# Kernel optimization log

Measured on AMD Instinct MI355X. Metric: run time of the kernel, lower is better.

The kernel has to match this reference:

```python
import jax, jax.numpy as jnp
import numpy as np

N = 50000      # nodes
E2 = 400000    # undirected edges
E = 2 * E2     # directed edges (each undirected edge in both directions)
DIN = 512      # input feature dim
DH = 128       # MLP hidden
C = 8          # num classes / BP channels


def setup_inputs() -> dict:
    key = jax.random.key(0)
    ks = jax.random.split(key, 9)
    x = jax.random.normal(ks[0], (N, DIN), jnp.float32)
    src0 = jax.random.randint(ks[1], (E2,), 0, N)
    dst0 = jax.random.randint(ks[2], (E2,), 0, N)
    # symmetric directed edge list: row 0 = source j, row 1 = target i
    edge_index = jnp.stack([jnp.concatenate([src0, dst0]),
                            jnp.concatenate([dst0, src0])])
    w0 = jax.random.uniform(ks[3], (E2,), jnp.float32, 0.5, 1.5)
    edge_weight = jnp.concatenate([w0, w0])  # reverse edge shares weight
    # edge_rv[e] = index of the reverse of edge e
    edge_rv = jnp.concatenate([jnp.arange(E2) + E2, jnp.arange(E2)])
    W1 = jax.random.normal(ks[4], (DIN, DH), jnp.float32) * 0.05
    b1 = jnp.zeros((DH,), jnp.float32)
    W2 = jax.random.normal(ks[5], (DH, C), jnp.float32) * 0.05
    b2 = jnp.zeros((C,), jnp.float32)
    param = jax.random.normal(ks[6], (C, C), jnp.float32) * 0.1
    return {"x": x, "edge_index": edge_index, "edge_weight": edge_weight,
            "edge_rv": edge_rv, "W1": W1, "b1": b1, "W2": W2, "b2": b2,
            "param": param, "K": 5}


def log_normalize(log_x):
    return log_x - jax.nn.logsumexp(log_x, axis=-1, keepdims=True)


def reference(x, edge_index, edge_weight, edge_rv, W1, b1, W2, b2, param, K):
    # MLP transform + LogSoftmax -> initial log-beliefs [N, C]
    h = jax.nn.relu(x @ W1 + b1)
    log_b0 = jax.nn.log_softmax(h @ W2 + b2, axis=-1)

    # learn_H=True: logH = logsigmoid(param + param^T), [C, C]
    logH = jax.nn.log_sigmoid(param + param.T)
    src, dst = edge_index[0], edge_index[1]
    # per-edge coupling matrix [E, C, C]
    logC = edge_weight[:, None, None] * logH[None, :, :]

    log_b = log_b0
    log_msg = None
    for _ in range(K):
        x_j = log_b[src]                       # gather source beliefs [E, C]
        if log_msg is not None:
            x_j = x_j - log_msg[edge_rv]       # remove reverse message
        # tropical-semiring matvec in log domain: logsumexp over source channel
        log_msg = log_normalize(jax.nn.logsumexp(x_j[:, :, None] + logC, axis=1))
        agg = jax.ops.segment_sum(log_msg, dst, num_segments=N)  # scatter-add
        log_b = log_normalize(log_b0 + agg)
    return log_b
```

## Files before the change

kernel.cpp:

```cpp
#include <hip/hip_runtime.h>
#include <hip/hip_bf16.h>
#include <math.h>

#define NN 50000
#define EE 800000
#define DINK 512
#define DHK 128
#define CK 8
#define KIT 5
#define NBLKS 196

typedef __attribute__((ext_vector_type(8))) short short8;
typedef __attribute__((ext_vector_type(4))) float f32x4;

__device__ __forceinline__ unsigned short f2bf(float f) {
    union { float f; unsigned int u; } v;
    v.f = f;
    unsigned int u = v.u;
    unsigned int r = (u + 0x7FFFu + ((u >> 16) & 1u)) >> 16;
    return (unsigned short)r;
}
__device__ __forceinline__ float bfu2f(unsigned int lo16) {
    union { unsigned int u; float f; } v;
    v.u = lo16 << 16;
    return v.f;
}

__global__ __launch_bounds__(64) void logH_kernel(const float* __restrict__ param,
                                                  float* __restrict__ logH) {
    int t = threadIdx.x;
    int i = t >> 3, j = t & 7;
    float z = param[i * 8 + j] + param[j * 8 + i];
    logH[t] = fminf(z, 0.0f) - log1pf(expf(-fabsf(z)));
}

__global__ __launch_bounds__(256) void w1t_kernel(const float* __restrict__ W1,
                                                  unsigned short* __restrict__ W1t) {
    int idx = blockIdx.x * 256 + threadIdx.x;
    int n = idx >> 9;
    int k = idx & 511;
    W1t[idx] = f2bf(W1[(size_t)k * DHK + n]);
}

__global__ __launch_bounds__(256) void mlp_mfma_kernel(
    const float* __restrict__ x, const unsigned short* __restrict__ W1t,
    const float* __restrict__ b1, const float* __restrict__ W2,
    const float* __restrict__ b2, float* __restrict__ logb0) {
    __shared__ unsigned short hs[128 * 136];
    __shared__ float W2s[128 * 8];
    __shared__ float b1s[128];
    __shared__ float b2s[8];

    const int tid = threadIdx.x;
    const int wave = tid >> 6;
    const int lane = tid & 63;
    const int q = lane >> 4;
    const int lm = lane & 15;
    const int wm = wave >> 1, wn = wave & 1;
    const int n0 = blockIdx.x * 128;

    if (tid < 128) b1s[tid] = b1[tid];
    if (tid < 8) b2s[tid] = b2[tid];
    {
        int i = tid * 4;
        *(float4*)&W2s[i] = *(const float4*)&W2[i];
    }
    __syncthreads();

    const float* xptr[4];
#pragma unroll
    for (int mt = 0; mt < 4; ++mt) {
        int r = n0 + wm * 64 + mt * 16 + lm;
        if (r > NN - 1) r = NN - 1;
        xptr[mt] = x + (size_t)r * DINK + q * 8;
    }
    const unsigned short* bptr[4];
#pragma unroll
    for (int nt = 0; nt < 4; ++nt) {
        int c = wn * 64 + nt * 16 + lm;
        bptr[nt] = W1t + (size_t)c * DINK + q * 8;
    }

    f32x4 acc[4][4];
#pragma unroll
    for (int mt = 0; mt < 4; ++mt)
#pragma unroll
        for (int nt = 0; nt < 4; ++nt) acc[mt][nt] = (f32x4){0.f, 0.f, 0.f, 0.f};

    float4 ar[4][2];
    short8 bc[4];
#pragma unroll
    for (int mt = 0; mt < 4; ++mt) {
        ar[mt][0] = *(const float4*)(xptr[mt]);
        ar[mt][1] = *(const float4*)(xptr[mt] + 4);
    }
#pragma unroll
    for (int nt = 0; nt < 4; ++nt) bc[nt] = *(const short8*)(bptr[nt]);

#pragma unroll
    for (int k0 = 32; k0 <= DINK; k0 += 32) {
        float4 ar2[4][2];
        short8 b2f[4];
        if (k0 < DINK) {
#pragma unroll
            for (int mt = 0; mt < 4; ++mt) {
                ar2[mt][0] = *(const float4*)(xptr[mt] + k0);
                ar2[mt][1] = *(const float4*)(xptr[mt] + k0 + 4);
            }
#pragma unroll
            for (int nt = 0; nt < 4; ++nt)
                b2f[nt] = *(const short8*)(bptr[nt] + k0);
        }
        short8 af[4];
#pragma unroll
        for (int mt = 0; mt < 4; ++mt) {
            union { short8 s; __hip_bfloat162 h[4]; } cv;
            cv.h[0] = __float22bfloat162_rn(make_float2(ar[mt][0].x, ar[mt][0].y));
            cv.h[1] = __float22bfloat162_rn(make_float2(ar[mt][0].z, ar[mt][0].w));
            cv.h[2] = __float22bfloat162_rn(make_float2(ar[mt][1].x, ar[mt][1].y));
            cv.h[3] = __float22bfloat162_rn(make_float2(ar[mt][1].z, ar[mt][1].w));
            af[mt] = cv.s;
        }
#pragma unroll
        for (int mt = 0; mt < 4; ++mt)
#pragma unroll
            for (int nt = 0; nt < 4; ++nt)
                acc[mt][nt] = __builtin_amdgcn_mfma_f32_16x16x32_bf16(
                    af[mt], bc[nt], acc[mt][nt], 0, 0, 0);
        if (k0 < DINK) {
#pragma unroll
            for (int mt = 0; mt < 4; ++mt) {
                ar[mt][0] = ar2[mt][0];
                ar[mt][1] = ar2[mt][1];
            }
#pragma unroll
            for (int nt = 0; nt < 4; ++nt) bc[nt] = b2f[nt];
        }
    }

#pragma unroll
    for (int nt = 0; nt < 4; ++nt) {
        int j = wn * 64 + nt * 16 + lm;
        float bj = b1s[j];
#pragma unroll
        for (int mt = 0; mt < 4; ++mt) {
            int rbase = wm * 64 + mt * 16 + q * 4;
#pragma unroll
            for (int r = 0; r < 4; ++r) {
                float h = fmaxf(acc[mt][nt][r] + bj, 0.0f);
                hs[(rbase + r) * 136 + j] = f2bf(h);
            }
        }
    }
    __syncthreads();

    int row = tid >> 1;
    int half = tid & 1;
    const unsigned short* hp = &hs[row * 136 + half * 64];
    float p[8] = {0.f, 0.f, 0.f, 0.f, 0.f, 0.f, 0.f, 0.f};
#pragma unroll
    for (int ch = 0; ch < 8; ++ch) {
        uint4 c4 = *(const uint4*)(hp + ch * 8);
        unsigned int uu[4] = {c4.x, c4.y, c4.z, c4.w};
#pragma unroll
        for (int p2 = 0; p2 < 4; ++p2) {
            float h0 = bfu2f(uu[p2] & 0xFFFFu);
            float h1 = bfu2f(uu[p2] >> 16);
            int j = half * 64 + ch * 8 + p2 * 2;
            const float* w0 = &W2s[j * 8];
            const float* w1 = &W2s[(j + 1) * 8];
#pragma unroll
            for (int c = 0; c < 8; ++c) p[c] = fmaf(h0, w0[c], p[c]);
#pragma unroll
            for (int c = 0; c < 8; ++c) p[c] = fmaf(h1, w1[c], p[c]);
        }
    }
#pragma unroll
    for (int c = 0; c < 8; ++c) p[c] += __shfl_xor(p[c], 1, 64);
    int grow = n0 + row;
    if (half == 0 && grow < NN) {
        float v[8];
        float mx = -1e30f;
#pragma unroll
        for (int c = 0; c < 8; ++c) {
            v[c] = p[c] + b2s[c];
            mx = fmaxf(mx, v[c]);
        }
        float s = 0.0f;
#pragma unroll
        for (int c = 0; c < 8; ++c) s += expf(v[c] - mx);
        float ln = mx + logf(s);
        float4* p0 = (float4*)&logb0[(size_t)grow * 8];
        p0[0] = make_float4(v[0] - ln, v[1] - ln, v[2] - ln, v[3] - ln);
        p0[1] = make_float4(v[4] - ln, v[5] - ln, v[6] - ln, v[7] - ln);
    }
}


__global__ __launch_bounds__(256) void deg_kernel(const int* __restrict__ dst,
                                                  int* __restrict__ cnt) {
    int e = blockIdx.x * 256 + threadIdx.x;
    if (e < EE) atomicAdd(&cnt[dst[e]], 1);
}

__global__ __launch_bounds__(256) void scan_partial_kernel(
    const int* __restrict__ cnt, int* __restrict__ partial) {
    __shared__ int sd[256];
    int t = threadIdx.x;
    int i = blockIdx.x * 256 + t;
    sd[t] = (i < NN) ? cnt[i] : 0;
    __syncthreads();
#pragma unroll
    for (int s = 128; s > 0; s >>= 1) {
        if (t < s) sd[t] += sd[t + s];
        __syncthreads();
    }
    if (t == 0) partial[blockIdx.x] = sd[0];
}

__global__ __launch_bounds__(256) void scan_tops_kernel(
    const int* __restrict__ partial, int* __restrict__ tops) {
    __shared__ int sd[256];
    int t = threadIdx.x;
    sd[t] = (t < NBLKS) ? partial[t] : 0;
    __syncthreads();
#pragma unroll
    for (int s = 1; s < 256; s <<= 1) {
        int a = sd[t];
        int b = (t >= s) ? sd[t - s] : 0;
        __syncthreads();
        sd[t] = a + b;
        __syncthreads();
    }
    if (t < NBLKS) tops[t] = (t > 0) ? sd[t - 1] : 0;
}

__global__ __launch_bounds__(256) void scan_write_kernel(
    const int* __restrict__ cnt, const int* __restrict__ tops,
    int* __restrict__ off) {
    __shared__ int sd[256];
    int t = threadIdx.x;
    int i = blockIdx.x * 256 + t;
    int v = (i < NN) ? cnt[i] : 0;
    sd[t] = v;
    __syncthreads();
#pragma unroll
    for (int s = 1; s < 256; s <<= 1) {
        int a = sd[t];
        int b = (t >= s) ? sd[t - s] : 0;
        __syncthreads();
        sd[t] = a + b;
        __syncthreads();
    }
    if (i < NN) off[i] = tops[blockIdx.x] + sd[t] - v;
    if (i == NN - 1) off[NN] = EE;
}

__global__ __launch_bounds__(256) void pos_kernel(
    const int* __restrict__ src, const int* __restrict__ dst,
    const float* __restrict__ ew, const int* __restrict__ off,
    int* __restrict__ cnt, int* __restrict__ pos,
    int2* __restrict__ perm_sw, int* __restrict__ perm_dst) {
    int e = blockIdx.x * 256 + threadIdx.x;
    if (e >= EE) return;
    int d = dst[e];
    int p = off[d] + atomicAdd(&cnt[d], 1);
    pos[e] = p;
    int2 sw;
    sw.x = src[e];
    sw.y = __float_as_int(ew[e]);
    perm_sw[p] = sw;
    perm_dst[p] = d;
}

__global__ __launch_bounds__(256) void rvpos_kernel(const int* __restrict__ rv,
                                                    const int* __restrict__ pos,
                                                    int* __restrict__ perm_rvp) {
    int e = blockIdx.x * 256 + threadIdx.x;
    if (e >= EE) return;
    perm_rvp[pos[e]] = pos[rv[e]];
}

__global__ __launch_bounds__(256) void init_xin_kernel(
    const int2* __restrict__ perm_sw, const float* __restrict__ logb0,
    float* __restrict__ xin, float* __restrict__ perm_w) {
    int p = blockIdx.x * 256 + threadIdx.x;
    if (p >= EE) return;
    int2 sw = perm_sw[p];
    perm_w[p] = __int_as_float(sw.y);
    const float4* pb = (const float4*)&logb0[(size_t)sw.x * 8];
    float4 a = pb[0], b = pb[1];
    float4* po = (float4*)&xin[(size_t)p * 8];
    po[0] = a;
    po[1] = b;
}


__global__ __launch_bounds__(256) void edge_msg_kernel(
    const float* __restrict__ perm_w, const float* __restrict__ logH,
    const float* __restrict__ xin, float* __restrict__ msg_out) {
    __shared__ float lH[64];
    if (threadIdx.x < 64) lH[threadIdx.x] = logH[threadIdx.x];
    __syncthreads();
    int p = blockIdx.x * 256 + threadIdx.x;
    if (p >= EE) return;

    float w = perm_w[p];
    const float4* pb = (const float4*)&xin[(size_t)p * 8];
    float4 v0 = pb[0], v1 = pb[1];
    float xj[8] = {v0.x, v0.y, v0.z, v0.w, v1.x, v1.y, v1.z, v1.w};

    float M = xj[0];
#pragma unroll
    for (int c = 1; c < 8; ++c) M = fmaxf(M, xj[c]);
#pragma unroll
    for (int c = 0; c < 8; ++c) xj[c] -= M;

    float mg[8];
#pragma unroll
    for (int c2 = 0; c2 < 8; ++c2) {
        float ssum = 0.0f;
#pragma unroll
        for (int c1 = 0; c1 < 8; ++c1)
            ssum += __expf(fmaf(w, lH[c1 * 8 + c2], xj[c1]));
        mg[c2] = M + __logf(ssum);
    }

    float4* po = (float4*)&msg_out[(size_t)p * 8];
    po[0] = make_float4(mg[0], mg[1], mg[2], mg[3]);
    po[1] = make_float4(mg[4], mg[5], mg[6], mg[7]);
}

__global__ __launch_bounds__(256) void node_belief_kernel(
    const float* __restrict__ logb0, const int* __restrict__ off,
    const float* __restrict__ msg, float* __restrict__ belief,
    float* __restrict__ out, int write_out) {
    int t = blockIdx.x * 256 + threadIdx.x;
    int n = t >> 3;
    int c = t & 7;
    if (n >= NN) return;
    int j0 = off[n], j1 = off[n + 1];
    float a = logb0[(size_t)n * 8 + c];
    for (int j = j0; j < j1; ++j) a += msg[(size_t)j * 8 + c];
    float mx = a;
#pragma unroll
    for (int s = 1; s < 8; s <<= 1) mx = fmaxf(mx, __shfl_xor(mx, s, 8));
    float ex = __expf(a - mx);
    float sum = ex;
#pragma unroll
    for (int s = 1; s < 8; s <<= 1) sum += __shfl_xor(sum, s, 8);
    float v = a - (mx + __logf(sum));
    if (write_out) out[(size_t)n * 8 + c] = v;
    else belief[(size_t)n * 8 + c] = v;
}

__global__ __launch_bounds__(256) void edge_scatter_kernel(
    const int* __restrict__ perm_dst, const int* __restrict__ perm_rvp,
    const float* __restrict__ belief, const float* __restrict__ msg,
    float* __restrict__ xin) {
    int p = blockIdx.x * 256 + threadIdx.x;
    if (p >= EE) return;
    int d = perm_dst[p];
    int r = perm_rvp[p];
    const float4* pb = (const float4*)&belief[(size_t)d * 8];
    float4 b0 = pb[0], b1 = pb[1];
    const float4* pm = (const float4*)&msg[(size_t)p * 8];
    float4 m0 = pm[0], m1 = pm[1];
    float4* po = (float4*)&xin[(size_t)r * 8];
    po[0] = make_float4(b0.x - m0.x, b0.y - m0.y, b0.z - m0.z, b0.w - m0.w);
    po[1] = make_float4(b1.x - m1.x, b1.y - m1.y, b1.z - m1.z, b1.w - m1.w);
}

extern "C" void kernel_launch(void* const* d_in, const int* in_sizes, int n_in,
                              void* d_out, int out_size, void* d_ws, size_t ws_size,
                              hipStream_t stream) {
    const float* x = (const float*)d_in[0];
    const int* ei = (const int*)d_in[1];
    const float* ew = (const float*)d_in[2];
    const int* rv = (const int*)d_in[3];
    const float* W1 = (const float*)d_in[4];
    const float* b1 = (const float*)d_in[5];
    const float* W2 = (const float*)d_in[6];
    const float* b2 = (const float*)d_in[7];
    const float* param = (const float*)d_in[8];
    float* out = (float*)d_out;

    const int* src = ei;
    const int* dst = ei + EE;

    float* wsf = (float*)d_ws;
    float* logH = wsf;
    float* logb0 = logH + 64;
    float* belief = logb0 + (size_t)NN * 8;
    float* msg = belief + (size_t)NN * 8;
    float* xin = msg + (size_t)EE * 8;
    float* perm_w = xin + (size_t)EE * 8;
    int* off = (int*)(perm_w + EE);
    int2* perm_sw = (int2*)(off + (NN + 1));
    int* perm_rvp = (int*)(perm_sw + EE);
    int* perm_dst = perm_rvp + EE;
    unsigned short* W1t = (unsigned short*)(perm_dst + EE);
    int* pos = (int*)xin;
    int* cnt = pos + EE;
    int* partial = cnt + NN;
    int* tops = partial + NBLKS;

    logH_kernel<<<1, 64, 0, stream>>>(param, logH);
    w1t_kernel<<<256, 256, 0, stream>>>(W1, W1t);
    mlp_mfma_kernel<<<(NN + 127) / 128, 256, 0, stream>>>(x, W1t, b1, W2, b2,
                                                          logb0);

    const int EB = (EE + 255) / 256;

    hipMemsetAsync(cnt, 0, (size_t)NN * sizeof(int), stream);
    deg_kernel<<<EB, 256, 0, stream>>>(dst, cnt);
    scan_partial_kernel<<<NBLKS, 256, 0, stream>>>(cnt, partial);
    scan_tops_kernel<<<1, 256, 0, stream>>>(partial, tops);
    scan_write_kernel<<<NBLKS, 256, 0, stream>>>(cnt, tops, off);
    hipMemsetAsync(cnt, 0, (size_t)NN * sizeof(int), stream);
    pos_kernel<<<EB, 256, 0, stream>>>(src, dst, ew, off, cnt, pos, perm_sw,
                                       perm_dst);
    rvpos_kernel<<<EB, 256, 0, stream>>>(rv, pos, perm_rvp);
    init_xin_kernel<<<EB, 256, 0, stream>>>(perm_sw, logb0, xin, perm_w);

    const int NB8 = (NN * 8 + 255) / 256;
    for (int it = 0; it < KIT; ++it) {
        int last = (it == KIT - 1) ? 1 : 0;
        edge_msg_kernel<<<EB, 256, 0, stream>>>(perm_w, logH, xin, msg);
        node_belief_kernel<<<NB8, 256, 0, stream>>>(logb0, off, msg, belief,
                                                    out, last);
        if (!last)
            edge_scatter_kernel<<<EB, 256, 0, stream>>>(perm_dst, perm_rvp,
                                                        belief, msg, xin);
    }
}
```

Measured before the change: 503.9 us.

## Fuse belief normalization with reverse-message scatter and drop init/prep kernels

Merges the node belief kernel and the edge scatter kernel into one per-node-block kernel. Each block keeps its 32 normalized beliefs in shared memory and scatters belief minus message to the reverse-edge slots for its contiguous CSR edge range. It also drops the init_xin kernel and the perm_w array by having the first edge_msg iteration gather logb0 directly and read the weight from perm_sw, and it merges the logH and W1 transpose prep kernels into one launch. The aim is fewer launches and no round-trip of beliefs through global memory. The cost is that the scatter loop's work per block varies with node degree, which can unbalance blocks.

```diff
diff --git a/kernel.cpp b/kernel.cpp
--- a/kernel.cpp
+++ b/kernel.cpp
@@ -9,6 +9,7 @@
 #define CK 8
 #define KIT 5
 #define NBLKS 196
+#define NPB 32
 
 typedef __attribute__((ext_vector_type(8))) short short8;
 typedef __attribute__((ext_vector_type(4))) float f32x4;
@@ -26,20 +27,20 @@
     return v.f;
 }
 
-__global__ __launch_bounds__(64) void logH_kernel(const float* __restrict__ param,
-                                                  float* __restrict__ logH) {
-    int t = threadIdx.x;
-    int i = t >> 3, j = t & 7;
-    float z = param[i * 8 + j] + param[j * 8 + i];
-    logH[t] = fminf(z, 0.0f) - log1pf(expf(-fabsf(z)));
-}
-
-__global__ __launch_bounds__(256) void w1t_kernel(const float* __restrict__ W1,
-                                                  unsigned short* __restrict__ W1t) {
-    int idx = blockIdx.x * 256 + threadIdx.x;
-    int n = idx >> 9;
-    int k = idx & 511;
-    W1t[idx] = f2bf(W1[(size_t)k * DHK + n]);
+__global__ __launch_bounds__(256) void prep_kernel(
+    const float* __restrict__ W1, const float* __restrict__ param,
+    unsigned short* __restrict__ W1t, float* __restrict__ logH) {
+    if (blockIdx.x < 256) {
+        int idx = blockIdx.x * 256 + threadIdx.x;
+        int n = idx >> 9;
+        int k = idx & 511;
+        W1t[idx] = f2bf(W1[(size_t)k * DHK + n]);
+    } else if (threadIdx.x < 64) {
+        int t = threadIdx.x;
+        int i = t >> 3, j = t & 7;
+        float z = param[i * 8 + j] + param[j * 8 + i];
+        logH[t] = fminf(z, 0.0f) - log1pf(expf(-fabsf(z)));
+    }
 }
 
 __global__ __launch_bounds__(256) void mlp_mfma_kernel(
@@ -281,32 +282,21 @@
     perm_rvp[pos[e]] = pos[rv[e]];
 }
 
-__global__ __launch_bounds__(256) void init_xin_kernel(
-    const int2* __restrict__ perm_sw, const float* __restrict__ logb0,
-    float* __restrict__ xin, float* __restrict__ perm_w) {
+
+__global__ __launch_bounds__(256) void edge_msg_kernel(
+    const int2* __restrict__ perm_sw, const float* __restrict__ logH,
+    const float* __restrict__ logb0, const float* __restrict__ xin,
+    float* __restrict__ msg_out, int first) {
+    __shared__ float lH[64];
+    if (threadIdx.x < 64) lH[threadIdx.x] = logH[threadIdx.x];
+    __syncthreads();
     int p = blockIdx.x * 256 + threadIdx.x;
     if (p >= EE) return;
+
     int2 sw = perm_sw[p];
-    perm_w[p] = __int_as_float(sw.y);
-    const float4* pb = (const float4*)&logb0[(size_t)sw.x * 8];
-    float4 a = pb[0], b = pb[1];
-    float4* po = (float4*)&xin[(size_t)p * 8];
-    po[0] = a;
-    po[1] = b;
-}
-
-
-__global__ __launch_bounds__(256) void edge_msg_kernel(
-    const float* __restrict__ perm_w, const float* __restrict__ logH,
-    const float* __restrict__ xin, float* __restrict__ msg_out) {
-    __shared__ float lH[64];
-    if (threadIdx.x < 64) lH[threadIdx.x] = logH[threadIdx.x];
-    __syncthreads();
-    int p = blockIdx.x * 256 + threadIdx.x;
-    if (p >= EE) return;
-
-    float w = perm_w[p];
-    const float4* pb = (const float4*)&xin[(size_t)p * 8];
+    float w = __int_as_float(sw.y);
+    const float4* pb = first ? (const float4*)&logb0[(size_t)sw.x * 8]
+                             : (const float4*)&xin[(size_t)p * 8];
     float4 v0 = pb[0], v1 = pb[1];
     float xj[8] = {v0.x, v0.y, v0.z, v0.w, v1.x, v1.y, v1.z, v1.w};
 
@@ -331,44 +321,46 @@
     po[1] = make_float4(mg[4], mg[5], mg[6], mg[7]);
 }
 
-__global__ __launch_bounds__(256) void node_belief_kernel(
+__global__ __launch_bounds__(256) void node_fused_kernel(
     const float* __restrict__ logb0, const int* __restrict__ off,
-    const float* __restrict__ msg, float* __restrict__ belief,
-    float* __restrict__ out, int write_out) {
-    int t = blockIdx.x * 256 + threadIdx.x;
-    int n = t >> 3;
-    int c = t & 7;
-    if (n >= NN) return;
-    int j0 = off[n], j1 = off[n + 1];
-    float a = logb0[(size_t)n * 8 + c];
-    for (int j = j0; j < j1; ++j) a += msg[(size_t)j * 8 + c];
-    float mx = a;
-#pragma unroll
-    for (int s = 1; s < 8; s <<= 1) mx = fmaxf(mx, __shfl_xor(mx, s, 8));
-    float ex = __expf(a - mx);
-    float sum = ex;
-#pragma unroll
-    for (int s = 1; s < 8; s <<= 1) sum += __shfl_xor(sum, s, 8);
-    float v = a - (mx + __logf(sum));
-    if (write_out) out[(size_t)n * 8 + c] = v;
-    else belief[(size_t)n * 8 + c] = v;
-}
-
-__global__ __launch_bounds__(256) void edge_scatter_kernel(
-    const int* __restrict__ perm_dst, const int* __restrict__ perm_rvp,
-    const float* __restrict__ belief, const float* __restrict__ msg,
-    float* __restrict__ xin) {
-    int p = blockIdx.x * 256 + threadIdx.x;
-    if (p >= EE) return;
-    int d = perm_dst[p];
-    int r = perm_rvp[p];
-    const float4* pb = (const float4*)&belief[(size_t)d * 8];
-    float4 b0 = pb[0], b1 = pb[1];
-    const float4* pm = (const float4*)&msg[(size_t)p * 8];
-    float4 m0 = pm[0], m1 = pm[1];
-    float4* po = (float4*)&xin[(size_t)r * 8];
-    po[0] = make_float4(b0.x - m0.x, b0.y - m0.y, b0.z - m0.z, b0.w - m0.w);
-    po[1] = make_float4(b1.x - m1.x, b1.y - m1.y, b1.z - m1.z, b1.w - m1.w);
+    const float* __restrict__ msg, const int* __restrict__ perm_dst,
+    const int* __restrict__ perm_rvp, float* __restrict__ xin,
+    float* __restrict__ out, int last) {
+    __shared__ float sb[NPB * 8];
+    const int n0 = blockIdx.x * NPB;
+    const int t = threadIdx.x;
+    const int nl = t >> 3;
+    const int c = t & 7;
+    const int n = n0 + nl;
+
+    if (n < NN) {
+        int j0 = off[n], j1 = off[n + 1];
+        float a = logb0[(size_t)n * 8 + c];
+        for (int j = j0; j < j1; ++j) a += msg[(size_t)j * 8 + c];
+        float mx = a;
+#pragma unroll
+        for (int s = 1; s < 8; s <<= 1) mx = fmaxf(mx, __shfl_xor(mx, s, 8));
+        float sum = __expf(a - mx);
+#pragma unroll
+        for (int s = 1; s < 8; s <<= 1) sum += __shfl_xor(sum, s, 8);
+        float v = a - (mx + __logf(sum));
+        if (last) out[(size_t)n * 8 + c] = v;
+        sb[nl * 8 + c] = v;
+    }
+    if (last) return;
+    __syncthreads();
+
+    const int nend = (n0 + NPB < NN) ? (n0 + NPB) : NN;
+    const int jb0 = off[n0];
+    const int jb1 = off[nend];
+    const int items = (jb1 - jb0) * 8;
+    for (int item = t; item < items; item += 256) {
+        int j = jb0 + (item >> 3);
+        int c2 = item & 7;
+        int dl = perm_dst[j] - n0;
+        float val = sb[dl * 8 + c2] - msg[(size_t)j * 8 + c2];
+        xin[(size_t)perm_rvp[j] * 8 + c2] = val;
+    }
 }
 
 extern "C" void kernel_launch(void* const* d_in, const int* in_sizes, int n_in,
@@ -391,11 +383,9 @@
     float* wsf = (float*)d_ws;
     float* logH = wsf;
     float* logb0 = logH + 64;
-    float* belief = logb0 + (size_t)NN * 8;
-    float* msg = belief + (size_t)NN * 8;
+    float* msg = logb0 + (size_t)NN * 8;
     float* xin = msg + (size_t)EE * 8;
-    float* perm_w = xin + (size_t)EE * 8;
-    int* off = (int*)(perm_w + EE);
+    int* off = (int*)(xin + (size_t)EE * 8);
     int2* perm_sw = (int2*)(off + (NN + 1));
     int* perm_rvp = (int*)(perm_sw + EE);
     int* perm_dst = perm_rvp + EE;
@@ -405,8 +395,7 @@
     int* partial = cnt + NN;
     int* tops = partial + NBLKS;
 
-    logH_kernel<<<1, 64, 0, stream>>>(param, logH);
-    w1t_kernel<<<256, 256, 0, stream>>>(W1, W1t);
+    prep_kernel<<<257, 256, 0, stream>>>(W1, param, W1t, logH);
     mlp_mfma_kernel<<<(NN + 127) / 128, 256, 0, stream>>>(x, W1t, b1, W2, b2,
                                                           logb0);
 
@@ -421,16 +410,14 @@
     pos_kernel<<<EB, 256, 0, stream>>>(src, dst, ew, off, cnt, pos, perm_sw,
                                        perm_dst);
     rvpos_kernel<<<EB, 256, 0, stream>>>(rv, pos, perm_rvp);
-    init_xin_kernel<<<EB, 256, 0, stream>>>(perm_sw, logb0, xin, perm_w);
-
-    const int NB8 = (NN * 8 + 255) / 256;
+
+    const int NB = (NN + NPB - 1) / NPB;
     for (int it = 0; it < KIT; ++it) {
+        int first = (it == 0) ? 1 : 0;
         int last = (it == KIT - 1) ? 1 : 0;
-        edge_msg_kernel<<<EB, 256, 0, stream>>>(perm_w, logH, xin, msg);
-        node_belief_kernel<<<NB8, 256, 0, stream>>>(logb0, off, msg, belief,
-                                                    out, last);
-        if (!last)
-            edge_scatter_kernel<<<EB, 256, 0, stream>>>(perm_dst, perm_rvp,
-                                                        belief, msg, xin);
-    }
-}
+        edge_msg_kernel<<<EB, 256, 0, stream>>>(perm_sw, logH, logb0, xin, msg,
+                                                first);
+        node_fused_kernel<<<NB, 256, 0, stream>>>(logb0, off, msg, perm_dst,
+                                                  perm_rvp, xin, out, last);
+    }
+}
```

New measurement: 486.1 us. 1.04x faster.
